# Performance work log

Measured on AMD Instinct MI355X. Metric: run time of the kernel, lower is better.

## Reference

```python
import jax, jax.numpy as jnp
import numpy as np
import math

INPUT_SIZE = 128  # feature dim D, from init_kwargs

def setup_inputs() -> dict:
    key = jax.random.key(0)
    k1, k2 = jax.random.split(key)
    B, N, D = 4, 4096, INPUT_SIZE
    inp = jax.random.normal(k1, (B, N, D), dtype=jnp.float32)
    adj = jax.random.randint(k2, (B, N, N), 0, 2, dtype=jnp.int32)
    return {"input": inp, "adj": adj}

def reference(input, adj):
    # scores: [B, N, N] = X X^T / sqrt(D)
    scores = jnp.matmul(input, jnp.swapaxes(input, 1, 2)) / math.sqrt(INPUT_SIZE)
    neg = jnp.asarray(-1e12, dtype=scores.dtype)
    masked = jnp.where(adj > 0, scores, neg)
    attention = jax.nn.softmax(masked, axis=2)
    out_hid = jnp.matmul(attention, input)  # [B, N, D]
    return out_hid
```

## Files before the change

kernel.cpp:

```cpp
#include <hip/hip_runtime.h>
#include <hip/hip_bf16.h>


#define NN 4096
#define DD 128
#define BK 128
#define NT (NN / BK)

#define XBT_REL 32768
#define BUF1_OFF 65536
#define PS_OFF 139264
#define LDS_BYTES (PS_OFF + 1024)

typedef __attribute__((ext_vector_type(8))) short bf16x8;
typedef __attribute__((ext_vector_type(16))) float f32x16;

static __device__ __forceinline__ unsigned f2bf(float f) {
    union { float f; unsigned u; } v; v.f = f;
    return (v.u + 0x7fffu + ((v.u >> 16) & 1u)) >> 16;
}

static __device__ __forceinline__ void gl_lds16(const void* g, void* l) {
    __builtin_amdgcn_global_load_lds(
        (const __attribute__((address_space(1))) unsigned*)g,
        (__attribute__((address_space(3))) unsigned*)l, 16, 0, 0);
}

static __device__ __forceinline__ unsigned cvtpk(float lo, float hi) {
    unsigned r;
    asm("v_cvt_pk_bf16_f32 %0, %1, %2" : "=v"(r) : "v"(lo), "v"(hi));
    return r;
}
static __device__ __forceinline__ void plswap(unsigned& a, unsigned& b) {
    asm volatile("v_permlane32_swap_b32 %0, %1" : "+v"(a), "+v"(b));
}

__global__ __launch_bounds__(256)
void gat_prep(const float* __restrict__ X, unsigned short* __restrict__ xb,
              unsigned short* __restrict__ xbt) {
    __shared__ unsigned short tile[64][132];
    const int t = threadIdx.x;
    const int b  = blockIdx.x >> 6;
    const int kc = blockIdx.x & 63;
    const float* src = X + ((size_t)b * NN + kc * 64) * DD;
    unsigned short* xbo = xb + ((size_t)b * NN + kc * 64) * DD;

    #pragma unroll
    for (int it = 0; it < 8; ++it) {
        int f = it * 256 + t;
        int k = f >> 5, d4 = (f & 31) * 4;
        float4 v = *(const float4*)(src + (size_t)f * 4);
        uint2 pk;
        pk.x = f2bf(v.x) | (f2bf(v.y) << 16);
        pk.y = f2bf(v.z) | (f2bf(v.w) << 16);
        *(uint2*)(xbo + (size_t)f * 4) = pk;
        *(uint2*)(&tile[k][d4]) = pk;
    }
    __syncthreads();
    const int d = t >> 1, kb0 = (t & 1) * 32;
    unsigned short* dst = xbt + (size_t)b * DD * NN + (size_t)d * NN + kc * 64 + kb0;
    #pragma unroll
    for (int c = 0; c < 4; ++c) {
        union { uint4 o; unsigned short e[8]; } u;
        #pragma unroll
        for (int j = 0; j < 8; ++j) u.e[j] = tile[kb0 + c * 8 + j][d];
        *(uint4*)(dst + c * 8) = u.o;
    }
}

__global__ __launch_bounds__(512, 2)
void gat_fused(const unsigned short* __restrict__ xb,
               const unsigned short* __restrict__ xbt,
               const int* __restrict__ adj,
               float* __restrict__ out) {
    extern __shared__ char lds[];
    const int t = threadIdx.x;
    const int w = t >> 6, l = t & 63;
    const int l32 = l & 31, h5 = l >> 5;
    const int rw = w >> 2;
    const int kh = w & 3;
    const int bid  = blockIdx.x;
    const int b    = bid >> 6;
    const int row0 = (bid & 63) * 64;
    const int qbase = row0 + rw * 32;
    const int kbase = kh * 32;

    const char* xb_b  = (const char*)(xb  + (size_t)b * NN * DD);
    const char* xbt_b = (const char*)(xbt + (size_t)b * DD * NN);
    const int*  Ag    = adj + (size_t)b * NN * NN;
    float*      Og    = out + (size_t)b * NN * DD;

    bf16x8 qfrag[8];
    {
        const char* qp = xb_b + (size_t)(qbase + l32) * 256;
        #pragma unroll
        for (int c = 0; c < 8; ++c)
            qfrag[c] = *(const bf16x8*)(qp + c * 32 + h5 * 16);
    }

    int off_xb[4], off_xbt[4];
    #pragma unroll
    for (int j = 0; j < 4; ++j) {
        int r = w * 16 + 4 * j + (l >> 4);
        off_xb[j]  = r * 256      + (((l & 15) ^ (r & 7)) * 16);
        off_xbt[j] = r * (NN * 2) + (((l & 15) ^ (r & 7)) * 16);
    }
    char* bufA = lds;
    char* bufB = lds + BUF1_OFF;
    const int* arow = Ag + (size_t)(qbase + l32) * NN + kbase + 4 * h5;

#define STAGE(BUF, KEY0) do {                                                  \
    _Pragma("unroll")                                                          \
    for (int j = 0; j < 4; ++j) {                                              \
        gl_lds16(xb_b  + (size_t)(KEY0) * 256 + off_xb[j],                     \
                 (BUF) + w * 4096 + j * 1024);                                 \
        gl_lds16(xbt_b + (size_t)(KEY0) * 2 + off_xbt[j],                      \
                 (BUF) + XBT_REL + w * 4096 + j * 1024);                       \
    }                                                                          \
} while (0)

    STAGE(bufA, 0);
    int4 avA[4], avB[4], avC[4];
    #pragma unroll
    for (int g = 0; g < 4; ++g) avA[g] = *(const int4*)(arow + g * 8);
    #pragma unroll
    for (int g = 0; g < 4; ++g) avB[g] = *(const int4*)(arow + BK + g * 8);

    f32x16 oacc[4];
    #pragma unroll
    for (int d = 0; d < 4; ++d) oacc[d] = (f32x16)(0.0f);
    float psum = 0.f;

#define COMPUTE(BUF, AV) do {                                                  \
    f32x16 sacc = (f32x16)(0.0f);                                              \
    {                                                                          \
        const int krow = kbase + l32;                                          \
        const char* kp = (BUF) + krow * 256;                                   \
        const int sw = krow & 7;                                               \
        _Pragma("unroll")                                                      \
        for (int c = 0; c < 8; ++c) {                                          \
            bf16x8 kf = *(const bf16x8*)(kp + (((2 * c + h5) ^ sw) * 16));     \
            sacc = __builtin_amdgcn_mfma_f32_32x32x16_bf16(                    \
                kf, qfrag[c], sacc, 0, 0, 0);                                  \
        }                                                                      \
    }                                                                          \
    float p[16];                                                               \
    {                                                                          \
        const float SC = 0.08838834764831845f;                \
        _Pragma("unroll")                                                      \
        for (int g = 0; g < 4; ++g) {                                          \
            int4 a = (AV)[g];                                                  \
            p[4*g+0] = (a.x > 0) ? __expf(sacc[4*g+0] * SC) : 0.f;             \
            p[4*g+1] = (a.y > 0) ? __expf(sacc[4*g+1] * SC) : 0.f;             \
            p[4*g+2] = (a.z > 0) ? __expf(sacc[4*g+2] * SC) : 0.f;             \
            p[4*g+3] = (a.w > 0) ? __expf(sacc[4*g+3] * SC) : 0.f;             \
            psum += p[4*g+0] + p[4*g+1] + p[4*g+2] + p[4*g+3];                 \
        }                                                                      \
    }                                                                          \
      \
      \
    union { bf16x8 v; unsigned u[4]; } pf0u, pf1u;                             \
    {                                                                          \
        unsigned a0 = cvtpk(p[0],  p[1]),  b0 = cvtpk(p[4],  p[5]);            \
        unsigned a1 = cvtpk(p[2],  p[3]),  b1 = cvtpk(p[6],  p[7]);            \
        plswap(a0, b0);  plswap(a1, b1);                                       \
        pf0u.u[0] = a0; pf0u.u[1] = a1; pf0u.u[2] = b0; pf0u.u[3] = b1;        \
        unsigned a2 = cvtpk(p[8],  p[9]),  b2 = cvtpk(p[12], p[13]);           \
        unsigned a3 = cvtpk(p[10], p[11]), b3 = cvtpk(p[14], p[15]);           \
        plswap(a2, b2);  plswap(a3, b3);                                       \
        pf1u.u[0] = a2; pf1u.u[1] = a3; pf1u.u[2] = b2; pf1u.u[3] = b3;        \
    }                                                                          \
    {                                                                          \
        _Pragma("unroll")                                                      \
        for (int db = 0; db < 4; ++db) {                                       \
            const int vrow = db * 32 + l32;                                    \
            const int swv = vrow & 7;                                          \
            const char* vp = (BUF) + XBT_REL + vrow * 256;                     \
            bf16x8 v0 = *(const bf16x8*)(vp + (((4 * kh + h5) ^ swv) * 16));   \
            oacc[db] = __builtin_amdgcn_mfma_f32_32x32x16_bf16(                \
                pf0u.v, v0, oacc[db], 0, 0, 0);                                \
            bf16x8 v1 = *(const bf16x8*)(vp + (((4 * kh + 2 + h5) ^ swv) * 16)); \
            oacc[db] = __builtin_amdgcn_mfma_f32_32x32x16_bf16(                \
                pf1u.v, v1, oacc[db], 0, 0, 0);                                \
        }                                                                      \
    }                                                                          \
} while (0)

    for (int kt = 0; kt < NT - 1; ++kt) {
        asm volatile("s_waitcnt vmcnt(4)" ::: "memory");
        __builtin_amdgcn_s_barrier();
        STAGE(bufB, (kt + 1) * BK);
        if (kt + 2 < NT) {
            #pragma unroll
            for (int g = 0; g < 4; ++g)
                avC[g] = *(const int4*)(arow + (kt + 2) * BK + g * 8);
        }
        COMPUTE(bufA, avA);
        char* tmp = bufA; bufA = bufB; bufB = tmp;
        #pragma unroll
        for (int g = 0; g < 4; ++g) { avA[g] = avB[g]; avB[g] = avC[g]; }
    }
    asm volatile("s_waitcnt vmcnt(0)" ::: "memory");
    __builtin_amdgcn_s_barrier();
    COMPUTE(bufA, avA);

    psum += __shfl_xor(psum, 32, 64);
    __syncthreads();

    float* slot = (float*)(lds + w * 17408);
    #pragma unroll
    for (int db = 0; db < 4; ++db)
        #pragma unroll
        for (int r = 0; r < 16; ++r) {
            const int lrow = (r & 3) + 8 * (r >> 2) + 4 * h5;
            slot[lrow * 136 + db * 32 + l32] = oacc[db][r];
        }
    float* psarea = (float*)(lds + PS_OFF);
    if (l < 32) psarea[w * 32 + l] = psum;
    __syncthreads();

    {
        const int R   = w * 8 + (l >> 3);
        const int q32 = R & 31, rwR = R >> 5;
        const int d0  = (l & 7) * 16;
        float tot = psarea[(rwR * 4 + 0) * 32 + q32]
                  + psarea[(rwR * 4 + 1) * 32 + q32]
                  + psarea[(rwR * 4 + 2) * 32 + q32]
                  + psarea[(rwR * 4 + 3) * 32 + q32];
        float invt = 1.0f / tot;
        float4 acc[4];
        #pragma unroll
        for (int j = 0; j < 4; ++j) acc[j] = (float4){0.f, 0.f, 0.f, 0.f};
        #pragma unroll
        for (int kx = 0; kx < 4; ++kx) {
            const float* sp = (const float*)(lds + (rwR * 4 + kx) * 17408)
                              + q32 * 136 + d0;
            #pragma unroll
            for (int j = 0; j < 4; ++j) {
                float4 v = *(const float4*)(sp + 4 * j);
                acc[j].x += v.x; acc[j].y += v.y;
                acc[j].z += v.z; acc[j].w += v.w;
            }
        }
        float* op = Og + (size_t)(row0 + R) * DD + d0;
        #pragma unroll
        for (int j = 0; j < 4; ++j) {
            float4 res;
            res.x = acc[j].x * invt; res.y = acc[j].y * invt;
            res.z = acc[j].z * invt; res.w = acc[j].w * invt;
            *(float4*)(op + 4 * j) = res;
        }
    }
#undef COMPUTE
#undef STAGE
}

extern "C" void kernel_launch(void* const* d_in, const int* in_sizes, int n_in,
                              void* d_out, int out_size, void* d_ws, size_t ws_size,
                              hipStream_t stream) {
    const float* X   = (const float*)d_in[0];
    const int*   adj = (const int*)d_in[1];
    float*       out = (float*)d_out;
    unsigned short* xb  = (unsigned short*)d_ws;
    unsigned short* xbt = xb + (size_t)4 * NN * DD;

    hipFuncSetAttribute((const void*)gat_fused,
                        hipFuncAttributeMaxDynamicSharedMemorySize, LDS_BYTES);
    gat_prep<<<dim3(256), dim3(256), 0, stream>>>(X, xb, xbt);
    gat_fused<<<dim3(256), dim3(512), LDS_BYTES, stream>>>(xb, xbt, adj, out);
}
```

Before: 395.2 us.

## Remap block order, widen LDS swizzle, and unroll double-buffer loop by two

The block index is remapped so that consecutive hardware block IDs, which are spread across XCDs, land on specific batch and row tiles. The goal is better L2 locality for the shared per-batch X tiles. The LDS XOR swizzle is widened from 3 to 4 bits on both the staging writes and the MFMA fragment reads, to cut bank conflicts on the 128-wide bf16 rows. The main loop is unrolled by two with fixed even/odd buffers, which removes the pointer and register rotation, but the adjacency prefetch distance drops from two tiles to one. That makes adj load latency more exposed.

```diff
diff --git a/kernel.cpp b/kernel.cpp
--- a/kernel.cpp
+++ b/kernel.cpp
@@ -79,7 +79,9 @@
     const int l32 = l & 31, h5 = l >> 5;
     const int rw = w >> 2;
     const int kh = w & 3;
-    const int bid  = blockIdx.x;
+
+    const int bid0 = blockIdx.x;
+    const int bid  = ((bid0 & 7) >> 1) * 64 + (bid0 & 1) * 32 + (bid0 >> 3);
     const int b    = bid >> 6;
     const int row0 = (bid & 63) * 64;
     const int qbase = row0 + rw * 32;
@@ -102,8 +104,8 @@
     #pragma unroll
     for (int j = 0; j < 4; ++j) {
         int r = w * 16 + 4 * j + (l >> 4);
-        off_xb[j]  = r * 256      + (((l & 15) ^ (r & 7)) * 16);
-        off_xbt[j] = r * (NN * 2) + (((l & 15) ^ (r & 7)) * 16);
+        off_xb[j]  = r * 256      + (((l & 15) ^ (r & 15)) * 16);
+        off_xbt[j] = r * (NN * 2) + (((l & 15) ^ (r & 15)) * 16);
     }
     char* bufA = lds;
     char* bufB = lds + BUF1_OFF;
@@ -119,12 +121,11 @@
     }                                                                          \
 } while (0)
 
-    STAGE(bufA, 0);
-    int4 avA[4], avB[4], avC[4];
-    #pragma unroll
-    for (int g = 0; g < 4; ++g) avA[g] = *(const int4*)(arow + g * 8);
-    #pragma unroll
-    for (int g = 0; g < 4; ++g) avB[g] = *(const int4*)(arow + BK + g * 8);
+#define LOAD_ADJ(AV, KT) do {                                                  \
+    _Pragma("unroll")                                                          \
+    for (int g = 0; g < 4; ++g)                                                \
+        (AV)[g] = *(const int4*)(arow + (size_t)(KT) * BK + g * 8);            \
+} while (0)
 
     f32x16 oacc[4];
     #pragma unroll
@@ -136,7 +137,7 @@
     {                                                                          \
         const int krow = kbase + l32;                                          \
         const char* kp = (BUF) + krow * 256;                                   \
-        const int sw = krow & 7;                                               \
+        const int sw = krow & 15;                                              \
         _Pragma("unroll")                                                      \
         for (int c = 0; c < 8; ++c) {                                          \
             bf16x8 kf = *(const bf16x8*)(kp + (((2 * c + h5) ^ sw) * 16));     \
@@ -157,8 +158,7 @@
             psum += p[4*g+0] + p[4*g+1] + p[4*g+2] + p[4*g+3];                 \
         }                                                                      \
     }                                                                          \
-      \
-      \
+         \
     union { bf16x8 v; unsigned u[4]; } pf0u, pf1u;                             \
     {                                                                          \
         unsigned a0 = cvtpk(p[0],  p[1]),  b0 = cvtpk(p[4],  p[5]);            \
@@ -174,7 +174,7 @@
         _Pragma("unroll")                                                      \
         for (int db = 0; db < 4; ++db) {                                       \
             const int vrow = db * 32 + l32;                                    \
-            const int swv = vrow & 7;                                          \
+            const int swv = vrow & 15;                                         \
             const char* vp = (BUF) + XBT_REL + vrow * 256;                     \
             bf16x8 v0 = *(const bf16x8*)(vp + (((4 * kh + h5) ^ swv) * 16));   \
             oacc[db] = __builtin_amdgcn_mfma_f32_32x32x16_bf16(                \
@@ -186,23 +186,32 @@
     }                                                                          \
 } while (0)
 
-    for (int kt = 0; kt < NT - 1; ++kt) {
+    STAGE(bufA, 0);
+    int4 avE[4], avO[4];
+    LOAD_ADJ(avE, 0);
+
+    for (int kt = 0; kt < NT - 2; kt += 2) {
+        LOAD_ADJ(avO, kt + 1);
         asm volatile("s_waitcnt vmcnt(4)" ::: "memory");
         __builtin_amdgcn_s_barrier();
         STAGE(bufB, (kt + 1) * BK);
-        if (kt + 2 < NT) {
-            #pragma unroll
-            for (int g = 0; g < 4; ++g)
-                avC[g] = *(const int4*)(arow + (kt + 2) * BK + g * 8);
-        }
-        COMPUTE(bufA, avA);
-        char* tmp = bufA; bufA = bufB; bufB = tmp;
-        #pragma unroll
-        for (int g = 0; g < 4; ++g) { avA[g] = avB[g]; avB[g] = avC[g]; }
-    }
+        COMPUTE(bufA, avE);
+
+        LOAD_ADJ(avE, kt + 2);
+        asm volatile("s_waitcnt vmcnt(4)" ::: "memory");
+        __builtin_amdgcn_s_barrier();
+        STAGE(bufA, (kt + 2) * BK);
+        COMPUTE(bufB, avO);
+    }
+    LOAD_ADJ(avO, NT - 1);
+    asm volatile("s_waitcnt vmcnt(4)" ::: "memory");
+    __builtin_amdgcn_s_barrier();
+    STAGE(bufB, (NT - 1) * BK);
+    COMPUTE(bufA, avE);
+
     asm volatile("s_waitcnt vmcnt(0)" ::: "memory");
     __builtin_amdgcn_s_barrier();
-    COMPUTE(bufA, avA);
+    COMPUTE(bufB, avO);
 
     psum += __shfl_xor(psum, 32, 64);
     __syncthreads();
@@ -253,6 +262,7 @@
     }
 #undef COMPUTE
 #undef STAGE
+#undef LOAD_ADJ
 }
 
 extern "C" void kernel_launch(void* const* d_in, const int* in_sizes, int n_in,
```

Measured after the change: 376.9 us. -4.6%, faster.
